# Optimization experiments

Measured on AMD Instinct MI355X. Metric: run time of the kernel, lower is better.

## Reference

```python
import jax, jax.numpy as jnp
import numpy as np

N = 131072
D = 1024
L = 128
B = 64  # number of bags / segments
TEMP = 1.0
EPS = 1e-12  # F.normalize eps


def setup_inputs() -> dict:
    key = jax.random.key(0)
    ks = jax.random.split(key, 5)
    feature = jax.random.normal(ks[0], (N, D), dtype=jnp.float32)
    batch = jnp.sort(jax.random.randint(ks[1], (N,), 0, B)).astype(jnp.int64)
    # xavier_normal_ std = sqrt(2 / (fan_in + fan_out))
    Wa = jax.random.normal(ks[2], (L, D), dtype=jnp.float32) * np.sqrt(2.0 / (D + L))
    Wb = jax.random.normal(ks[3], (L, D), dtype=jnp.float32) * np.sqrt(2.0 / (D + L))
    Wc = jax.random.normal(ks[4], (1, L), dtype=jnp.float32) * np.sqrt(2.0 / (L + 1))
    ba = jnp.zeros((L,), dtype=jnp.float32)
    bb = jnp.zeros((L,), dtype=jnp.float32)
    bc = jnp.zeros((1,), dtype=jnp.float32)
    return {"feature": feature, "batch": batch, "Wa": Wa, "ba": ba,
            "Wb": Wb, "bb": bb, "Wc": Wc, "bc": bc}


def reference(feature, batch, Wa, ba, Wb, bb, Wc, bc):
    # F.normalize: L2-normalize each row
    norm = jnp.linalg.norm(feature, axis=1, keepdims=True)
    feature = feature / jnp.maximum(norm, EPS)

    # gated attention score
    a = jax.nn.sigmoid(feature @ Wa.T + ba)            # [N, L]
    b = jnp.tanh(feature @ Wb.T + bb)                  # [N, L]
    score = ((a * b) @ Wc.T + bc) / TEMP               # [N, 1]

    # segment softmax over bags (torch_geometric softmax(score, batch))
    s = score[:, 0]                                    # [N]
    seg_max = jax.ops.segment_max(s, batch, num_segments=B)
    e = jnp.exp(s - seg_max[batch])
    denom = jax.ops.segment_sum(e, batch, num_segments=B)
    score = (e / denom[batch])[:, None]                # [N, 1]

    # scatter-sum pooling (dropout omitted: eval-mode determinism)
    out = jax.ops.segment_sum(score * feature, batch, num_segments=B)  # [B, D]
    return (out, score, feature)
```

## Files before the change

kernel.cpp:

```cpp
#include <hip/hip_runtime.h>
#include <hip/hip_bf16.h>
#include <cstdint>
#include <cstddef>

#define NROWS 131072
#define DDIM  1024
#define LDIM  128
#define BSEG  64
#define FIX2  281474976710656.0

typedef float f32x4 __attribute__((ext_vector_type(4)));
typedef short short8 __attribute__((ext_vector_type(8)));

__device__ inline unsigned short f2bf(float f) {
    union { float f; unsigned u; } x; x.f = f;
    unsigned u = x.u + 0x7fffu + ((x.u >> 16) & 1u);
    return (unsigned short)(u >> 16);
}

__device__ inline int lower_bound_dev(const int* __restrict__ arr, int n, int v) {
    int lo = 0, hi = n;
    while (lo < hi) { int mid = (lo + hi) >> 1; if (arr[mid] < v) lo = mid + 1; else hi = mid; }
    return lo;
}

__global__ void wconv_kernel(const float* __restrict__ Wa, const float* __restrict__ Wb,
                             unsigned short* __restrict__ wpre) {
    int n  = blockIdx.x;
    int kt = threadIdx.x >> 4;
    int q  = threadIdx.x & 15;
    const float* wrow = (n < LDIM) ? (Wa + (size_t)n * DDIM)
                                   : (Wb + (size_t)(n - LDIM) * DDIM);
    float4 v = *(const float4*)(wrow + kt * 64 + q * 4);
    ushort4 h;
    h.x = f2bf(v.x); h.y = f2bf(v.y); h.z = f2bf(v.z); h.w = f2bf(v.w);
    int w, nfi, rA;
    if (n < LDIM) { w = n >> 4; nfi = 0; rA = n & 15; }
    else { int m = n - LDIM; w = m >> 4; nfi = 1; rA = m & 15; }
    int kk    = q >> 3;
    int e     = (q & 7) * 4;
    int kl    = e >> 3;
    int inner = (e & 7) * 2;
    int lane  = kl * 16 + rA;
    int f     = ((kt * 2 + kk) * 8 + w) * 2 + nfi;
    *(ushort4*)((char*)wpre + f * 1024 + lane * 16 + inner) = h;
}

__global__ __launch_bounds__(512, 6)
void gemm_kernel(const float* __restrict__ feat, const unsigned short* __restrict__ wpre,
                 const float* __restrict__ ba, const float* __restrict__ bb,
                 const float* __restrict__ Wc, const float* __restrict__ bc,
                 const int* __restrict__ batch,
                 float* __restrict__ nf_out, float* __restrict__ s_out,
                 unsigned long long* __restrict__ acc64)
{
    __shared__ __align__(16) char smem[35584];
    float* invA_l = (float*)(smem + 32768);
    float* part   = (float*)(smem + 33024);
    float* u_row  = (float*)(smem + 35072);
    int*   seg_l  = (int*)(smem + 35328);

    const int tid  = threadIdx.x;
    const int w    = tid >> 6;
    const int lane = tid & 63;
    const int rblk = blockIdx.x * 64;
    const int sr   = tid >> 3;
    const int sc8  = tid & 7;

    if (tid < 64) seg_l[tid] = batch[rblk + tid];

    const float4* rowp4 = (const float4*)(feat + (size_t)(rblk + sr) * DDIM);

    f32x4 acc[4][2];
    #pragma unroll
    for (int i = 0; i < 4; ++i)
        #pragma unroll
        for (int j = 0; j < 2; ++j)
            acc[i][j] = (f32x4){0.f, 0.f, 0.f, 0.f};

    const int rA  = lane & 15;
    const int kl  = lane >> 4;
    const int swz = (lane & 7) << 4;
    const char* wsrc = (const char*)wpre + w * 2048 + lane * 16;

    float4 av1_0, av1_1, av2_0, av2_1;
    float sq = 0.f;

    #pragma unroll
    for (int j = 0; j < 2; ++j) {
        int cf = sc8 + j * 8;
        float4 v = rowp4[cf];
        sq += v.x * v.x + v.y * v.y + v.z * v.z + v.w * v.w;
        union { ushort4 h; __hip_bfloat162 b2[2]; } cv;
        cv.b2[0] = __float22bfloat162_rn(make_float2(v.x, v.y));
        cv.b2[1] = __float22bfloat162_rn(make_float2(v.z, v.w));
        *(ushort4*)(smem + ((sr * 128 + cf * 8) ^ ((sr & 7) << 4))) = cv.h;
    }
    av1_0 = rowp4[16 + sc8];
    av1_1 = rowp4[16 + sc8 + 8];
    __syncthreads();

    int cur = 0;
    for (int kt = 0; kt < 16; ++kt) {
        short8 wf[4];
        #pragma unroll
        for (int q = 0; q < 4; ++q)
            wf[q] = *(const short8*)(wsrc + (size_t)kt * 32768 + (q >> 1) * 16384 + (q & 1) * 1024);
        if (kt < 14) {
            av2_0 = rowp4[(kt + 2) * 16 + sc8];
            av2_1 = rowp4[(kt + 2) * 16 + sc8 + 8];
        }
        {
            const char* Abuf = smem + cur * 16384;
            #pragma unroll
            for (int kk = 0; kk < 2; ++kk) {
                int koff = (kk * 64 + kl * 16) ^ swz;
                #pragma unroll
                for (int mf = 0; mf < 4; ++mf) {
                    short8 af = *(const short8*)(Abuf + (mf * 16 + rA) * 128 + koff);
                    #pragma unroll
                    for (int nfi = 0; nfi < 2; ++nfi)
                        acc[mf][nfi] = __builtin_amdgcn_mfma_f32_16x16x32_bf16(
                            af, wf[kk * 2 + nfi], acc[mf][nfi], 0, 0, 0);
                }
            }
        }
        if (kt < 15) {
            char* Ab2 = smem + (cur ^ 1) * 16384;
            #pragma unroll
            for (int j = 0; j < 2; ++j) {
                int cf = sc8 + j * 8;
                float4 v = (j == 0) ? av1_0 : av1_1;
                sq += v.x * v.x + v.y * v.y + v.z * v.z + v.w * v.w;
                union { ushort4 h; __hip_bfloat162 b2[2]; } cv;
                cv.b2[0] = __float22bfloat162_rn(make_float2(v.x, v.y));
                cv.b2[1] = __float22bfloat162_rn(make_float2(v.z, v.w));
                *(ushort4*)(Ab2 + ((sr * 128 + cf * 8) ^ ((sr & 7) << 4))) = cv.h;
            }
        }
        __syncthreads();
        cur ^= 1;
        av1_0 = av2_0; av1_1 = av2_1;
    }

    sq += __shfl_xor(sq, 1, 64);
    sq += __shfl_xor(sq, 2, 64);
    sq += __shfl_xor(sq, 4, 64);
    if (sc8 == 0) invA_l[sr] = 1.f / fmaxf(sqrtf(sq), 1e-12f);
    __syncthreads();

    {
        int l0 = w * 16 + rA;
        float ba0 = ba[l0], bb0 = bb[l0], wc0 = Wc[l0];
        float vals[4][4];
        #pragma unroll
        for (int mf = 0; mf < 4; ++mf)
            #pragma unroll
            for (int reg = 0; reg < 4; ++reg) {
                int r = mf * 16 + kl * 4 + reg;
                float ia = invA_l[r];
                float pa0 = acc[mf][0][reg] * ia + ba0;
                float pb0 = acc[mf][1][reg] * ia + bb0;
                float a0 = 1.f / (1.f + __expf(-pa0));
                float b0 = 1.f - 2.f / (1.f + __expf(2.f * pb0));
                vals[mf][reg] = a0 * b0 * wc0;
            }
        #pragma unroll
        for (int mf = 0; mf < 4; ++mf)
            #pragma unroll
            for (int reg = 0; reg < 4; ++reg) {
                float v = vals[mf][reg];
                v += __shfl_xor(v, 1, 64);
                v += __shfl_xor(v, 2, 64);
                v += __shfl_xor(v, 4, 64);
                v += __shfl_xor(v, 8, 64);
                vals[mf][reg] = v;
            }
        if (rA == 0) {
            #pragma unroll
            for (int mf = 0; mf < 4; ++mf)
                #pragma unroll
                for (int reg = 0; reg < 4; ++reg)
                    part[w * 64 + mf * 16 + kl * 4 + reg] = vals[mf][reg];
        }
    }
    __syncthreads();
    if (tid < 64) {
        float s = part[tid] + part[64 + tid] + part[128 + tid] + part[192 + tid]
                + part[256 + tid] + part[320 + tid] + part[384 + tid] + part[448 + tid] + bc[0];
        u_row[tid] = __expf(s);
        s_out[rblk + tid] = s;
    }
    __syncthreads();

    {
        const int col = tid & 255;
        const int grp = tid >> 8;
        const float4* __restrict__ fbase = (const float4*)(feat + (size_t)rblk * DDIM);
        float4*       __restrict__ nbase = (float4*)(nf_out + (size_t)rblk * DDIM);
        float ax = 0.f, ay = 0.f, az = 0.f, aw = 0.f;
        int curseg = seg_l[grp];
        for (int rr = 0; rr < 8; ++rr) {
            int r0 = rr * 8 + grp;
            float4 v0 = fbase[(r0 + 0) * 256 + col];
            float4 v1 = fbase[(r0 + 2) * 256 + col];
            float4 v2 = fbase[(r0 + 4) * 256 + col];
            float4 v3 = fbase[(r0 + 6) * 256 + col];
            #pragma unroll
            for (int j = 0; j < 4; ++j) {
                int r = r0 + j * 2;
                float4 v = (j == 0) ? v0 : (j == 1) ? v1 : (j == 2) ? v2 : v3;
                int sg = seg_l[r];
                if (sg != curseg) {
                    unsigned long long* dst = acc64 + (size_t)curseg * DDIM + col * 4;
                    atomicAdd(&dst[0], (unsigned long long)(long long)((double)ax * FIX2));
                    atomicAdd(&dst[1], (unsigned long long)(long long)((double)ay * FIX2));
                    atomicAdd(&dst[2], (unsigned long long)(long long)((double)az * FIX2));
                    atomicAdd(&dst[3], (unsigned long long)(long long)((double)aw * FIX2));
                    ax = ay = az = aw = 0.f;
                    curseg = sg;
                }
                float ia = invA_l[r];
                float u  = u_row[r];
                v.x *= ia; v.y *= ia; v.z *= ia; v.w *= ia;
                nbase[r * 256 + col] = v;
                ax += u * v.x; ay += u * v.y; az += u * v.z; aw += u * v.w;
            }
        }
        unsigned long long* dst = acc64 + (size_t)curseg * DDIM + col * 4;
        atomicAdd(&dst[0], (unsigned long long)(long long)((double)ax * FIX2));
        atomicAdd(&dst[1], (unsigned long long)(long long)((double)ay * FIX2));
        atomicAdd(&dst[2], (unsigned long long)(long long)((double)az * FIX2));
        atomicAdd(&dst[3], (unsigned long long)(long long)((double)aw * FIX2));
    }
}

__global__ void softmax_kernel(const int* __restrict__ batch, float* __restrict__ score,
                               float* __restrict__ smax, float* __restrict__ ssum) {
    int b = blockIdx.x;
    int tid = threadIdx.x;
    int start = lower_bound_dev(batch, NROWS, b);
    int end   = lower_bound_dev(batch, NROWS, b + 1);
    __shared__ float red[4];
    __shared__ float bm, bd;

    float m = -INFINITY;
    for (int i = start + tid; i < end; i += 256) m = fmaxf(m, score[i]);
    #pragma unroll
    for (int k = 1; k < 64; k <<= 1) m = fmaxf(m, __shfl_xor(m, k, 64));
    if ((tid & 63) == 0) red[tid >> 6] = m;
    __syncthreads();
    if (tid == 0) bm = fmaxf(fmaxf(red[0], red[1]), fmaxf(red[2], red[3]));
    __syncthreads();
    float M = bm;

    float sum = 0.f;
    for (int i = start + tid; i < end; i += 256) sum += __expf(score[i] - M);
    #pragma unroll
    for (int k = 1; k < 64; k <<= 1) sum += __shfl_xor(sum, k, 64);
    if ((tid & 63) == 0) red[tid >> 6] = sum;
    __syncthreads();
    if (tid == 0) { bd = red[0] + red[1] + red[2] + red[3]; smax[b] = bm; ssum[b] = bd; }
    __syncthreads();
    float invD = 1.f / bd;

    for (int i = start + tid; i < end; i += 256)
        score[i] = __expf(score[i] - M) * invD;
}

__global__ void finalize_kernel(const unsigned long long* __restrict__ acc64,
                                const float* __restrict__ smax, const float* __restrict__ ssum,
                                float* __restrict__ out) {
    int i = blockIdx.x * 256 + threadIdx.x;
    int b = i >> 10;
    double denom = exp((double)smax[b]) * (double)ssum[b];
    out[i] = (float)(((double)(long long)acc64[i]) * (1.0 / FIX2) / denom);
}

extern "C" void kernel_launch(void* const* d_in, const int* in_sizes, int n_in,
                              void* d_out, int out_size, void* d_ws, size_t ws_size,
                              hipStream_t stream) {
    const float* feat  = (const float*)d_in[0];
    const int*   batch = (const int*)d_in[1];
    const float* Wa = (const float*)d_in[2];
    const float* ba = (const float*)d_in[3];
    const float* Wb = (const float*)d_in[4];
    const float* bb = (const float*)d_in[5];
    const float* Wc = (const float*)d_in[6];
    const float* bc = (const float*)d_in[7];

    float* out_seg = (float*)d_out;
    float* score   = out_seg + (size_t)BSEG * DDIM;
    float* nf      = score + NROWS;

    unsigned short*     wpre  = (unsigned short*)d_ws;
    unsigned long long* acc64 = (unsigned long long*)((char*)d_ws + 524288);
    float* smax = (float*)d_ws;
    float* ssum = smax + BSEG;

    hipMemsetAsync(acc64, 0, (size_t)BSEG * DDIM * 8, stream);
    wconv_kernel<<<256, 256, 0, stream>>>(Wa, Wb, wpre);
    gemm_kernel<<<NROWS / 64, 512, 0, stream>>>(feat, wpre, ba, bb, Wc, bc, batch,
                                                nf, score, acc64);
    softmax_kernel<<<BSEG, 256, 0, stream>>>(batch, score, smax, ssum);
    finalize_kernel<<<BSEG * DDIM / 256, 256, 0, stream>>>(acc64, smax, ssum, out_seg);
}
```

Baseline: 353.5 us.

## Retile GEMM waves into a 2x4 grid and shrink LDS double-buffer

Each of the 8 waves now computes a 32-row by 32-column tile of both the sigmoid and tanh projections, in a 2x4 row/column wave grid, instead of all 64 rows by 16 columns. This halves the A-fragment LDS reads per wave and doubles the weight-fragment global loads per wave. The weight prepack layout is reordered to match the new tile shape. The LDS double-buffer stride drops from 16 KB to the 8 KB each buffer actually needs, so total shared memory falls from about 35.5 KB to 19 KB and more blocks can fit per CU. The score reduction across waves is adjusted to sum four partials per row instead of eight.

```diff
diff --git a/kernel.cpp b/kernel.cpp
--- a/kernel.cpp
+++ b/kernel.cpp
@@ -34,15 +34,15 @@
     float4 v = *(const float4*)(wrow + kt * 64 + q * 4);
     ushort4 h;
     h.x = f2bf(v.x); h.y = f2bf(v.y); h.z = f2bf(v.z); h.w = f2bf(v.w);
-    int w, nfi, rA;
-    if (n < LDIM) { w = n >> 4; nfi = 0; rA = n & 15; }
-    else { int m = n - LDIM; w = m >> 4; nfi = 1; rA = m & 15; }
+    int wc, nfi, rA;
+    if (n < LDIM) { wc = n >> 5; nfi = (n >> 4) & 1; rA = n & 15; }
+    else { int m = n - LDIM; wc = m >> 5; nfi = 2 + ((m >> 4) & 1); rA = m & 15; }
     int kk    = q >> 3;
     int e     = (q & 7) * 4;
     int kl    = e >> 3;
     int inner = (e & 7) * 2;
     int lane  = kl * 16 + rA;
-    int f     = ((kt * 2 + kk) * 8 + w) * 2 + nfi;
+    int f     = ((kt * 2 + kk) * 4 + wc) * 4 + nfi;
     *(ushort4*)((char*)wpre + f * 1024 + lane * 16 + inner) = h;
 }
 
@@ -54,11 +54,11 @@
                  float* __restrict__ nf_out, float* __restrict__ s_out,
                  unsigned long long* __restrict__ acc64)
 {
-    __shared__ __align__(16) char smem[35584];
-    float* invA_l = (float*)(smem + 32768);
-    float* part   = (float*)(smem + 33024);
-    float* u_row  = (float*)(smem + 35072);
-    int*   seg_l  = (int*)(smem + 35328);
+    __shared__ __align__(16) char smem[19456];
+    float* invA_l = (float*)(smem + 16384);
+    float* part   = (float*)(smem + 16640);
+    float* u_row  = (float*)(smem + 18688);
+    int*   seg_l  = (int*)(smem + 18944);
 
     const int tid  = threadIdx.x;
     const int w    = tid >> 6;
@@ -66,22 +66,24 @@
     const int rblk = blockIdx.x * 64;
     const int sr   = tid >> 3;
     const int sc8  = tid & 7;
+    const int wr   = w >> 2;
+    const int wc   = w & 3;
+    const int rA   = lane & 15;
+    const int kl   = lane >> 4;
+    const int swz  = (rA & 7) << 4;
 
     if (tid < 64) seg_l[tid] = batch[rblk + tid];
 
     const float4* rowp4 = (const float4*)(feat + (size_t)(rblk + sr) * DDIM);
 
-    f32x4 acc[4][2];
+    f32x4 acc[2][4];
     #pragma unroll
-    for (int i = 0; i < 4; ++i)
+    for (int i = 0; i < 2; ++i)
         #pragma unroll
-        for (int j = 0; j < 2; ++j)
+        for (int j = 0; j < 4; ++j)
             acc[i][j] = (f32x4){0.f, 0.f, 0.f, 0.f};
 
-    const int rA  = lane & 15;
-    const int kl  = lane >> 4;
-    const int swz = (lane & 7) << 4;
-    const char* wsrc = (const char*)wpre + w * 2048 + lane * 16;
+    const char* wsrc = (const char*)wpre + wc * 4096 + lane * 16;
 
     float4 av1_0, av1_1, av2_0, av2_1;
     float sq = 0.f;
@@ -102,31 +104,32 @@
 
     int cur = 0;
     for (int kt = 0; kt < 16; ++kt) {
-        short8 wf[4];
+        short8 wf[8];
         #pragma unroll
-        for (int q = 0; q < 4; ++q)
-            wf[q] = *(const short8*)(wsrc + (size_t)kt * 32768 + (q >> 1) * 16384 + (q & 1) * 1024);
+        for (int q = 0; q < 8; ++q)
+            wf[q] = *(const short8*)(wsrc + (size_t)kt * 32768 + (q >> 2) * 16384 + (q & 3) * 1024);
         if (kt < 14) {
             av2_0 = rowp4[(kt + 2) * 16 + sc8];
             av2_1 = rowp4[(kt + 2) * 16 + sc8 + 8];
         }
         {
-            const char* Abuf = smem + cur * 16384;
+            const char* Abuf = smem + cur * 8192;
             #pragma unroll
             for (int kk = 0; kk < 2; ++kk) {
                 int koff = (kk * 64 + kl * 16) ^ swz;
                 #pragma unroll
-                for (int mf = 0; mf < 4; ++mf) {
-                    short8 af = *(const short8*)(Abuf + (mf * 16 + rA) * 128 + koff);
+                for (int mf = 0; mf < 2; ++mf) {
+                    int row = wr * 32 + mf * 16 + rA;
+                    short8 af = *(const short8*)(Abuf + row * 128 + koff);
                     #pragma unroll
-                    for (int nfi = 0; nfi < 2; ++nfi)
+                    for (int nfi = 0; nfi < 4; ++nfi)
                         acc[mf][nfi] = __builtin_amdgcn_mfma_f32_16x16x32_bf16(
-                            af, wf[kk * 2 + nfi], acc[mf][nfi], 0, 0, 0);
+                            af, wf[kk * 4 + nfi], acc[mf][nfi], 0, 0, 0);
                 }
             }
         }
         if (kt < 15) {
-            char* Ab2 = smem + (cur ^ 1) * 16384;
+            char* Ab2 = smem + (cur ^ 1) * 8192;
             #pragma unroll
             for (int j = 0; j < 2; ++j) {
                 int cf = sc8 + j * 8;
@@ -150,23 +153,28 @@
     __syncthreads();
 
     {
-        int l0 = w * 16 + rA;
-        float ba0 = ba[l0], bb0 = bb[l0], wc0 = Wc[l0];
-        float vals[4][4];
+        int l0 = wc * 32 + rA, l1 = l0 + 16;
+        float ba0 = ba[l0], ba1 = ba[l1], bb0 = bb[l0], bb1 = bb[l1];
+        float wc0 = Wc[l0], wc1 = Wc[l1];
+        float vals[2][4];
         #pragma unroll
-        for (int mf = 0; mf < 4; ++mf)
+        for (int mf = 0; mf < 2; ++mf)
             #pragma unroll
             for (int reg = 0; reg < 4; ++reg) {
-                int r = mf * 16 + kl * 4 + reg;
+                int r = wr * 32 + mf * 16 + kl * 4 + reg;
                 float ia = invA_l[r];
                 float pa0 = acc[mf][0][reg] * ia + ba0;
-                float pb0 = acc[mf][1][reg] * ia + bb0;
+                float pa1 = acc[mf][1][reg] * ia + ba1;
+                float pb0 = acc[mf][2][reg] * ia + bb0;
+                float pb1 = acc[mf][3][reg] * ia + bb1;
                 float a0 = 1.f / (1.f + __expf(-pa0));
                 float b0 = 1.f - 2.f / (1.f + __expf(2.f * pb0));
-                vals[mf][reg] = a0 * b0 * wc0;
+                float a1 = 1.f / (1.f + __expf(-pa1));
+                float b1 = 1.f - 2.f / (1.f + __expf(2.f * pb1));
+                vals[mf][reg] = a0 * b0 * wc0 + a1 * b1 * wc1;
             }
         #pragma unroll
-        for (int mf = 0; mf < 4; ++mf)
+        for (int mf = 0; mf < 2; ++mf)
             #pragma unroll
             for (int reg = 0; reg < 4; ++reg) {
                 float v = vals[mf][reg];
@@ -178,16 +186,17 @@
             }
         if (rA == 0) {
             #pragma unroll
-            for (int mf = 0; mf < 4; ++mf)
+            for (int mf = 0; mf < 2; ++mf)
                 #pragma unroll
                 for (int reg = 0; reg < 4; ++reg)
-                    part[w * 64 + mf * 16 + kl * 4 + reg] = vals[mf][reg];
+                    part[w * 64 + wr * 32 + mf * 16 + kl * 4 + reg] = vals[mf][reg];
         }
     }
     __syncthreads();
     if (tid < 64) {
-        float s = part[tid] + part[64 + tid] + part[128 + tid] + part[192 + tid]
-                + part[256 + tid] + part[320 + tid] + part[384 + tid] + part[448 + tid] + bc[0];
+        int wrr = tid >> 5;
+        float s = part[(wrr * 4 + 0) * 64 + tid] + part[(wrr * 4 + 1) * 64 + tid]
+                + part[(wrr * 4 + 2) * 64 + tid] + part[(wrr * 4 + 3) * 64 + tid] + bc[0];
         u_row[tid] = __expf(s);
         s_out[rblk + tid] = s;
     }
```

Measured after the change: 762.5 us. +115.7%, slower.
